# Performance work log

Measured on AMD Instinct MI355X. Metric: run time of the kernel, lower is better.

## Reference

```python
import jax, jax.numpy as jnp
import numpy as np

# dimensions (match init_kwargs / input_specs)
K = 25        # number of observation events
N_PER = 2048  # observations per event
B = 4096      # batch (sample_idx length)
D = 64        # input_dim
NDIM = 8      # memory_dim
H = D * NDIM  # hidden = 512
STEPS = 2     # euler ODE steps between consecutive obs_times
DT = 0.01
LOG_SQRT_2PI = 0.9189385332046727  # log(sqrt(2*pi))


def _xavier(key, shape):
    lim = np.sqrt(6.0 / (shape[0] + shape[1])).astype(np.float32)
    return jax.random.uniform(key, shape, jnp.float32, -lim, lim)


def setup_inputs() -> dict:
    key = jax.random.key(0)
    ks = jax.random.split(key, 10)
    # unique per-event indices (matches torch scatter-assign semantics)
    rng = np.random.RandomState(0)
    batch_idx = jnp.asarray(
        np.stack([rng.permutation(B)[:N_PER] for _ in range(K)]).reshape(-1),
        jnp.int32)
    return {
        "obs_times": jnp.arange(1, K + 1, dtype=jnp.float32) * (STEPS * DT),
        "event_pt": jnp.arange(K + 1, dtype=jnp.int32) * N_PER,
        "sample_idx": jnp.arange(B, dtype=jnp.int32),
        "X": jax.random.normal(ks[0], (K * N_PER, D), jnp.float32),
        "M": (jax.random.uniform(ks[1], (K * N_PER, D)) < 0.8).astype(jnp.float32),
        "batch_idx": batch_idx,
        # ODEFunc: Linear(H,H) -> Tanh -> Linear(H,H)
        "W_ode1": _xavier(ks[2], (H, H)), "b_ode1": jnp.zeros((H,), jnp.float32),
        "W_ode2": _xavier(ks[3], (H, H)), "b_ode2": jnp.zeros((H,), jnp.float32),
        # GRUCell(D, H)
        "W_ih": _xavier(ks[4], (3 * H, D)), "W_hh": _xavier(ks[5], (3 * H, H)),
        "b_ih": jnp.zeros((3 * H,), jnp.float32), "b_hh": jnp.zeros((3 * H,), jnp.float32),
        # p_model: Linear(H,H) -> ReLU -> (dropout=0) -> Linear(H, 2D)
        "Wp1": _xavier(ks[6], (H, H)), "bp1": jnp.zeros((H,), jnp.float32),
        "Wp2": _xavier(ks[7], (2 * D, H)), "bp2": jnp.zeros((2 * D,), jnp.float32),
    }


def reference(obs_times, event_pt, sample_idx, X, M, batch_idx,
              W_ode1, b_ode1, W_ode2, b_ode2,
              W_ih, W_hh, b_ih, b_hh, Wp1, bp1, Wp2, bp2):
    Xr = X.reshape(K, N_PER, D)
    Mr = M.reshape(K, N_PER, D)
    idx = batch_idx.reshape(K, N_PER)

    def ode_func(h):  # Linear -> Tanh -> Linear
        return jnp.tanh(h @ W_ode1.T + b_ode1) @ W_ode2.T + b_ode2

    def gru(x, h):  # torch GRUCell
        gi = x @ W_ih.T + b_ih
        gh = h @ W_hh.T + b_hh
        i_r, i_z, i_n = jnp.split(gi, 3, axis=1)
        h_r, h_z, h_n = jnp.split(gh, 3, axis=1)
        r = jax.nn.sigmoid(i_r + h_r)
        z = jax.nn.sigmoid(i_z + h_z)
        n = jnp.tanh(i_n + r * h_n)
        return (1.0 - z) * n + z * h

    def event_step(carry, inp):
        h, loss, m_tot = carry
        X_obs, M_obs, i_obs = inp
        # euler odeint over [0, dt], STEPS times to reach obs_time
        for _ in range(STEPS):
            h = h + DT * ode_func(h)
        # likelihood head on all samples, gather observed ones
        p = jax.nn.relu(h @ Wp1.T + bp1) @ Wp2.T + bp2       # [B, 2D]
        p_obs = p[i_obs]                                      # [N_PER, 2D]
        mean, logvar = jnp.split(p_obs, 2, axis=1)
        sigma = jnp.exp(0.5 * logvar)
        error = (X_obs - mean) / sigma
        losses = 0.5 * ((error * error + logvar + 2.0 * LOG_SQRT_2PI) * M_obs)
        # GRU update only on observed indices (scatter)
        h = h.at[i_obs].set(gru(X_obs, h[i_obs]))
        return (h, loss + losses.sum(), m_tot + M_obs.sum()), None

    h0 = jnp.zeros((B, H), jnp.float32)
    (h, loss, m_tot), _ = jax.lax.scan(event_step, (h0, jnp.float32(0.0), jnp.float32(0.0)), (Xr, Mr, idx))
    return (loss / m_tot, jnp.float32(0.0))
```

## Files before the change

### kernel.cpp

```cpp
#include <hip/hip_runtime.h>
#include <cstdint>
#include <cstddef>

#define BATCH 4096
#define DIM 64
#define HID 512
#define NPER 2048
#define KEV 25
#define DT_C 0.01f
#define LOG_SQRT_2PI_C 0.9189385332046727f

typedef __attribute__((ext_vector_type(8))) short short8;
typedef __attribute__((ext_vector_type(4))) float f32x4;

#define MFMA(a, b, c) __builtin_amdgcn_mfma_f32_16x16x32_bf16(a, b, c, 0, 0, 0)
#define BARRIER() __builtin_amdgcn_s_barrier()
#define SCHED0()  __builtin_amdgcn_sched_barrier(0)

__device__ __forceinline__ ushort f2bf(float f) {
    uint32_t u = __float_as_uint(f);
    u += 0x7FFF + ((u >> 16) & 1);
    return (ushort)(u >> 16);
}
__device__ __forceinline__ float sigmoidf_(float x) { return 1.0f / (1.0f + expf(-x)); }

__device__ __forceinline__ void gload_lds16(const ushort* g, ushort* l) {
    __builtin_amdgcn_global_load_lds(
        (const __attribute__((address_space(1))) void*)g,
        (__attribute__((address_space(3))) void*)l, 16, 0, 0);
}
__device__ __forceinline__ void wait_vm(int n) {
    if (n == 4)      asm volatile("s_waitcnt vmcnt(4)" ::: "memory");
    else if (n == 6) asm volatile("s_waitcnt vmcnt(6)" ::: "memory");
    else             asm volatile("s_waitcnt vmcnt(0)" ::: "memory");
}

__device__ __forceinline__ short8 frag64(const ushort* lds, int row, int ks, int lane) {
    int slot = ((ks << 2) + (lane >> 4)) ^ (row & 7);
    return *(const short8*)&lds[row * 64 + slot * 8];
}

__device__ __forceinline__ void gemm64_pipe(
    ushort* A0, ushort* A1, ushort* B0, ushort* B1,
    int w, int lane, int wr, int wc,
    const ushort* gA0, const ushort* gA1,
    const ushort* gB0, const ushort* gB1,
    const ushort* tA0, const ushort* tA1,
    const ushort* tB0, const ushort* tB1,
    int NT, bool tailToX, f32x4 acc[2][2], f32x4 accX[2][2])
{
    auto stage = [&](int b, int p) {
        ushort* A = b ? A1 : A0; ushort* B = b ? B1 : B0;
        if (p < 8) {
            gload_lds16(gA0 + (size_t)p * 64, &A[(w * 16) * 64]);
            gload_lds16(gA1 + (size_t)p * 64, &A[(w * 16 + 8) * 64]);
            gload_lds16(gB0 + (size_t)p * 64, &B[(w * 16) * 64]);
            gload_lds16(gB1 + (size_t)p * 64, &B[(w * 16 + 8) * 64]);
        } else {
            gload_lds16(tA0, &A[(w * 16) * 64]);
            gload_lds16(tA1, &A[(w * 16 + 8) * 64]);
            gload_lds16(tB0, &B[(w * 16) * 64]);
            gload_lds16(tB1, &B[(w * 16 + 8) * 64]);
        }
    };
    stage(0, 0);
    stage(1, 1);
    for (int t = 0; t < NT; ++t) {
        wait_vm((t + 1 < NT) ? 4 : 0);
        BARRIER();
        SCHED0();
        const ushort* Ab = (t & 1) ? A1 : A0;
        const ushort* Bb = (t & 1) ? B1 : B0;
        short8 af[2][2], bf[2][2];
        #pragma unroll
        for (int mi = 0; mi < 2; ++mi) {
            int r = wr * 32 + mi * 16 + (lane & 15);
            af[mi][0] = frag64(Ab, r, 0, lane);
            af[mi][1] = frag64(Ab, r, 1, lane);
        }
        #pragma unroll
        for (int ni = 0; ni < 2; ++ni) {
            int c = wc * 32 + ni * 16 + (lane & 15);
            bf[ni][0] = frag64(Bb, c, 0, lane);
            bf[ni][1] = frag64(Bb, c, 1, lane);
        }
        const bool toX = tailToX && (t == 8);
        #pragma unroll
        for (int ks = 0; ks < 2; ++ks)
            #pragma unroll
            for (int mi = 0; mi < 2; ++mi)
                #pragma unroll
                for (int ni = 0; ni < 2; ++ni) {
                    f32x4& a = toX ? accX[mi][ni] : acc[mi][ni];
                    a = MFMA(af[mi][ks], bf[ni][ks], a);
                }
        SCHED0();
        BARRIER();
        if (t + 2 < NT) stage(t & 1, t + 2);
    }
}

__global__ __launch_bounds__(256) void fuse1(
    const ushort* __restrict__ hb, const ushort* __restrict__ W1,
    const float* __restrict__ b1, ushort* __restrict__ tbb,
    const ushort* __restrict__ hgb, const ushort* __restrict__ Wp1,
    const float* __restrict__ bp1, ushort* __restrict__ qb, int mode)
{
    __shared__ __align__(16) ushort Alds[2][4096];
    __shared__ __align__(16) ushort Blds[2][4096];
    const int tid = threadIdx.x, lane = tid & 63, w = tid >> 6;
    const int wr = w >> 1, wc = w & 1;
    const int srow = lane >> 3, sg = ((lane & 7) ^ srow) << 3;
    const int bid = blockIdx.x;

    bool isQ; int b;
    if (mode == 2)        { isQ = true;  b = bid; }
    else if (bid < 512)   { isQ = false; b = bid; }
    else                  { isQ = true;  b = bid - 512; }
    const ushort* A = isQ ? hgb : hb;
    const ushort* W = isQ ? Wp1 : W1;
    const float* bias = isQ ? bp1 : b1;
    const int r0 = (b >> 3) * 64, c0 = (b & 7) * 64;

    f32x4 acc[2][2] = {}; f32x4 accX[2][2];
    gemm64_pipe(Alds[0], Alds[1], Blds[0], Blds[1], w, lane, wr, wc,
        A + (size_t)(r0 + w * 16 + srow) * HID + sg,
        A + (size_t)(r0 + w * 16 + 8 + srow) * HID + sg,
        W + (size_t)(c0 + w * 16 + srow) * HID + sg,
        W + (size_t)(c0 + w * 16 + 8 + srow) * HID + sg,
        nullptr, nullptr, nullptr, nullptr, 8, false, acc, accX);

    #pragma unroll
    for (int mi = 0; mi < 2; ++mi)
        #pragma unroll
        for (int ni = 0; ni < 2; ++ni) {
            const int c = c0 + wc * 32 + ni * 16 + (lane & 15);
            const float bv = bias[c];
            #pragma unroll
            for (int ii = 0; ii < 4; ++ii) {
                const int r = r0 + wr * 32 + mi * 16 + ((lane >> 4) << 2) + ii;
                const size_t o = (size_t)r * HID + c;
                float v = acc[mi][ni][ii] + bv;
                if (!isQ) tbb[o] = f2bf(tanhf(v));
                else      qb[o]  = f2bf(fmaxf(v, 0.0f));
            }
        }
}

__global__ __launch_bounds__(256) void fuse2(
    const ushort* __restrict__ tbb, const ushort* __restrict__ W2,
    const float* __restrict__ b2, float* __restrict__ h, ushort* __restrict__ hb,
    const ushort* __restrict__ qb, const ushort* __restrict__ Wp2,
    const float* __restrict__ bp2, const float* __restrict__ Xp,
    const float* __restrict__ Mp, float* __restrict__ sums, int mode)
{
    __shared__ __align__(16) ushort smem[24576];
    const int tid = threadIdx.x, lane = tid & 63, w = tid >> 6;
    const int wr = w >> 1, wc = w & 1;
    const int srow = lane >> 3, sg = ((lane & 7) ^ srow) << 3;
    const int bid = blockIdx.x;

    bool isP; int b;
    if (mode == 2)      { isP = true;  b = bid; }
    else if (bid < 512) { isP = false; b = bid; }
    else                { isP = true;  b = bid - 512; }

    if (!isP) {
        const int r0 = (b >> 3) * 64, c0 = (b & 7) * 64;
        ushort* A0 = smem;        ushort* A1 = smem + 4096;
        ushort* B0 = smem + 8192; ushort* B1 = smem + 12288;
        f32x4 acc[2][2] = {}; f32x4 accX[2][2];
        gemm64_pipe(A0, A1, B0, B1, w, lane, wr, wc,
            tbb + (size_t)(r0 + w * 16 + srow) * HID + sg,
            tbb + (size_t)(r0 + w * 16 + 8 + srow) * HID + sg,
            W2 + (size_t)(c0 + w * 16 + srow) * HID + sg,
            W2 + (size_t)(c0 + w * 16 + 8 + srow) * HID + sg,
            nullptr, nullptr, nullptr, nullptr, 8, false, acc, accX);
        #pragma unroll
        for (int mi = 0; mi < 2; ++mi)
            #pragma unroll
            for (int ni = 0; ni < 2; ++ni) {
                const int c = c0 + wc * 32 + ni * 16 + (lane & 15);
                const float bv = b2[c];
                #pragma unroll
                for (int ii = 0; ii < 4; ++ii) {
                    const int r = r0 + wr * 32 + mi * 16 + ((lane >> 4) << 2) + ii;
                    const size_t o = (size_t)r * HID + c;
                    float nh = h[o] + DT_C * (acc[mi][ni][ii] + bv);
                    h[o] = nh; hb[o] = f2bf(nh);
                }
            }
        return;
    }

    ushort* A0 = smem;        ushort* A1 = smem + 4096;
    ushort* B0 = smem + 8192; ushort* B1 = smem + 16384;
    const int r0t = b * 64;
    const int arow = w * 16 + srow;

    auto stage = [&](int bb, int k0) {
        ushort* A = bb ? A1 : A0; ushort* B = bb ? B1 : B0;
        gload_lds16(qb + (size_t)(r0t + arow) * HID + k0 + sg, &A[(w * 16) * 64]);
        gload_lds16(qb + (size_t)(r0t + arow + 8) * HID + k0 + sg, &A[(w * 16 + 8) * 64]);
        #pragma unroll
        for (int j = 0; j < 4; ++j) {
            int g = w * 4 + j;
            int rw = g * 8 + srow;
            gload_lds16(Wp2 + (size_t)rw * HID + k0 + (((lane & 7) ^ (rw & 7)) << 3),
                        &B[g * 8 * 64]);
        }
    };
    f32x4 acc[2][4] = {};
    stage(0, 0);
    stage(1, 64);
    for (int t = 0; t < 8; ++t) {
        wait_vm((t < 7) ? 6 : 0);
        BARRIER();
        SCHED0();
        const ushort* Ab = (t & 1) ? A1 : A0;
        const ushort* Bb = (t & 1) ? B1 : B0;
        short8 af[2][2], bf[4][2];
        #pragma unroll
        for (int mi = 0; mi < 2; ++mi) {
            int r = wr * 32 + mi * 16 + (lane & 15);
            af[mi][0] = frag64(Ab, r, 0, lane);
            af[mi][1] = frag64(Ab, r, 1, lane);
        }
        #pragma unroll
        for (int ni = 0; ni < 4; ++ni) {
            int c = wc * 64 + ni * 16 + (lane & 15);
            bf[ni][0] = frag64(Bb, c, 0, lane);
            bf[ni][1] = frag64(Bb, c, 1, lane);
        }
        #pragma unroll
        for (int ks = 0; ks < 2; ++ks)
            #pragma unroll
            for (int mi = 0; mi < 2; ++mi)
                #pragma unroll
                for (int ni = 0; ni < 4; ++ni)
                    acc[mi][ni] = MFMA(af[mi][ks], bf[ni][ks], acc[mi][ni]);
        SCHED0();
        BARRIER();
        if (t + 2 < 8) stage(t & 1, (t + 2) * 64);
    }

    float* Plds = (float*)smem;
    #pragma unroll
    for (int mi = 0; mi < 2; ++mi)
        #pragma unroll
        for (int ni = 0; ni < 4; ++ni) {
            int c = wc * 64 + ni * 16 + (lane & 15);
            float bv = bp2[c];
            #pragma unroll
            for (int ii = 0; ii < 4; ++ii) {
                int r = wr * 32 + mi * 16 + ((lane >> 4) << 2) + ii;
                Plds[r * 128 + c] = acc[mi][ni][ii] + bv;
            }
        }
    __syncthreads();

    float local = 0.0f;
    for (int t = tid; t < 64 * 64; t += 256) {
        int r = t >> 6, jj = t & 63;
        float mean = Plds[r * 128 + jj];
        float lv   = Plds[r * 128 + 64 + jj];
        int g = r0t + r;
        float err = (Xp[(size_t)g * 64 + jj] - mean) * expf(-0.5f * lv);
        local += 0.5f * (err * err + lv + 2.0f * LOG_SQRT_2PI_C) * Mp[(size_t)g * 64 + jj];
    }
    #pragma unroll
    for (int o = 32; o > 0; o >>= 1) local += __shfl_down(local, o);
    if (lane == 0) atomicAdd(sums, local);
}

__global__ __launch_bounds__(256) void fuse5(
    const ushort* __restrict__ hb, const ushort* __restrict__ Xbk,
    const int* __restrict__ idx,
    const ushort* __restrict__ Whh, const ushort* __restrict__ Wih,
    const float* __restrict__ bih, const float* __restrict__ bhh,
    float* __restrict__ rz, float* __restrict__ nh_, float* __restrict__ nx_,
    ushort* __restrict__ hgb)
{
    __shared__ __align__(16) ushort Alds[2][4096];
    __shared__ __align__(16) ushort Blds[2][4096];
    const int tid = threadIdx.x, lane = tid & 63, w = tid >> 6;
    const int wr = w >> 1, wc = w & 1;
    const int srow = lane >> 3, sg = ((lane & 7) ^ srow) << 3;
    const int bid = blockIdx.x;

    if (bid >= 768) {
        int t0 = (bid - 768) * 256 + tid;
        #pragma unroll
        for (int i = 0; i < 32; ++i) {
            int v = t0 + i * 4096;
            int row = v >> 6, c8 = (v & 63) << 3;
            size_t src = (size_t)idx[row] * HID + c8;
            size_t dst = (size_t)row * HID + c8;
            *(ushort4*)&hgb[dst]     = *(const ushort4*)&hb[src];
            *(ushort4*)&hgb[dst + 4] = *(const ushort4*)&hb[src + 4];
        }
        return;
    }

    int r0t, c0;
    const ushort *Bh, *Bx;
    bool tailX;
    if (bid < 512) { r0t = (bid >> 4) * 64; c0 = (bid & 15) * 64; Bh = Whh; Bx = Wih; tailX = false; }
    else { int t3 = bid - 512; r0t = (t3 >> 3) * 64; c0 = (t3 & 7) * 64;
           Bh = Whh + (size_t)1024 * HID; Bx = Wih + (size_t)1024 * DIM; tailX = true; }

    const int ar0 = r0t + w * 16 + srow, ar1 = r0t + w * 16 + 8 + srow;
    f32x4 acc[2][2] = {}, accX[2][2] = {};
    gemm64_pipe(Alds[0], Alds[1], Blds[0], Blds[1], w, lane, wr, wc,
        hb + (size_t)idx[ar0] * HID + sg,
        hb + (size_t)idx[ar1] * HID + sg,
        Bh + (size_t)(c0 + w * 16 + srow) * HID + sg,
        Bh + (size_t)(c0 + w * 16 + 8 + srow) * HID + sg,
        Xbk + (size_t)ar0 * DIM + sg,
        Xbk + (size_t)ar1 * DIM + sg,
        Bx + (size_t)(c0 + w * 16 + srow) * DIM + sg,
        Bx + (size_t)(c0 + w * 16 + 8 + srow) * DIM + sg,
        9, tailX, acc, accX);

    #pragma unroll
    for (int mi = 0; mi < 2; ++mi)
        #pragma unroll
        for (int ni = 0; ni < 2; ++ni) {
            const int c = c0 + wc * 32 + ni * 16 + (lane & 15);
            #pragma unroll
            for (int ii = 0; ii < 4; ++ii) {
                const int iobs = r0t + wr * 32 + mi * 16 + ((lane >> 4) << 2) + ii;
                if (!tailX) {
                    rz[(size_t)iobs * 1024 + c] =
                        sigmoidf_(acc[mi][ni][ii] + bih[c] + bhh[c]);
                } else {
                    nh_[(size_t)iobs * HID + c] = acc[mi][ni][ii] + bhh[1024 + c];
                    nx_[(size_t)iobs * HID + c] = accX[mi][ni][ii] + bih[1024 + c];
                }
            }
        }
}

__global__ __launch_bounds__(256) void combine_kernel(
    const float* __restrict__ rz, const float* __restrict__ nh_,
    const float* __restrict__ nx_, const int* __restrict__ idx,
    float* __restrict__ h, ushort* __restrict__ hb)
{
    int t = blockIdx.x * 256 + threadIdx.x;
    #pragma unroll
    for (int i = 0; i < 4; ++i) {
        int v = t + i * 65536;
        int row = v >> 7, j4 = (v & 127) << 2;
        float4 rr = *(const float4*)&rz[(size_t)row * 1024 + j4];
        float4 zz = *(const float4*)&rz[(size_t)row * 1024 + 512 + j4];
        float4 hn = *(const float4*)&nh_[(size_t)row * HID + j4];
        float4 xn = *(const float4*)&nx_[(size_t)row * HID + j4];
        size_t o = (size_t)idx[row] * HID + j4;
        float4 hv = *(const float4*)&h[o];
        float4 res; ushort4 ob;
        #define C1(c) { float n = tanhf(xn.c + rr.c * hn.c); \
                        res.c = (1.0f - zz.c) * n + zz.c * hv.c; ob.c = f2bf(res.c); }
        C1(x) C1(y) C1(z) C1(w)
        #undef C1
        *(float4*)&h[o] = res;
        *(ushort4*)&hb[o] = ob;
    }
}

__device__ __forceinline__ void block_atomic_sum(float v, float* acc) {
    __shared__ float red[4];
    #pragma unroll
    for (int off = 32; off > 0; off >>= 1) v += __shfl_down(v, off);
    int lane = threadIdx.x & 63, wid = threadIdx.x >> 6;
    if (lane == 0) red[wid] = v;
    __syncthreads();
    if (threadIdx.x == 0) atomicAdd(acc, red[0] + red[1] + red[2] + red[3]);
}

__global__ __launch_bounds__(256) void f2b4_kernel(
    const float* __restrict__ s, ushort* __restrict__ d, int n4)
{
    int t = blockIdx.x * 256 + threadIdx.x;
    if (t >= n4) return;
    float4 v = ((const float4*)s)[t];
    ushort4 o; o.x = f2bf(v.x); o.y = f2bf(v.y); o.z = f2bf(v.z); o.w = f2bf(v.w);
    ((ushort4*)d)[t] = o;
}

__global__ __launch_bounds__(256) void msum_kernel(
    const float* __restrict__ M, int n, float* __restrict__ m_acc)
{
    float v = 0.0f;
    for (int t = blockIdx.x * 256 + threadIdx.x; t < n; t += gridDim.x * 256)
        v += M[t];
    block_atomic_sum(v, m_acc);
}

__global__ void finalize_kernel(const float* __restrict__ sums, float* __restrict__ out) {
    if (threadIdx.x == 0) { out[0] = sums[0] / sums[1]; out[1] = 0.0f; }
}

extern "C" void kernel_launch(void* const* d_in, const int* in_sizes, int n_in,
                              void* d_out, int out_size, void* d_ws, size_t ws_size,
                              hipStream_t stream) {
    const float* X      = (const float*)d_in[3];
    const float* M      = (const float*)d_in[4];
    const int* batch_idx= (const int*)  d_in[5];
    const float* W_ode1 = (const float*)d_in[6];
    const float* b_ode1 = (const float*)d_in[7];
    const float* W_ode2 = (const float*)d_in[8];
    const float* b_ode2 = (const float*)d_in[9];
    const float* W_ih   = (const float*)d_in[10];
    const float* W_hh   = (const float*)d_in[11];
    const float* b_ih   = (const float*)d_in[12];
    const float* b_hh   = (const float*)d_in[13];
    const float* Wp1    = (const float*)d_in[14];
    const float* bp1    = (const float*)d_in[15];
    const float* Wp2    = (const float*)d_in[16];
    const float* bp2    = (const float*)d_in[17];
    float* out = (float*)d_out;

    float* ws    = (float*)d_ws;
    float* h     = ws;
    float* rz    = h   + (size_t)BATCH * HID;
    float* nh_   = rz  + (size_t)NPER * 1024;
    float* nx_   = nh_ + (size_t)NPER * HID;
    float* sums  = nx_ + (size_t)NPER * HID;
    ushort* hb   = (ushort*)(sums + 16);
    ushort* tbb  = hb  + (size_t)BATCH * HID;
    ushort* qb   = tbb + (size_t)BATCH * HID;
    ushort* hgb  = qb  + (size_t)NPER * HID;
    ushort* Xb   = hgb + (size_t)NPER * HID;
    ushort* W1b  = Xb  + (size_t)KEV * NPER * DIM;
    ushort* W2b  = W1b + (size_t)HID * HID;
    ushort* Wp1b = W2b + (size_t)HID * HID;
    ushort* Wp2b = Wp1b + (size_t)HID * HID;
    ushort* Wihb = Wp2b + (size_t)2 * DIM * HID;
    ushort* Whhb = Wihb + (size_t)3 * HID * DIM;

    hipMemsetAsync(h,    0, (size_t)BATCH * HID * sizeof(float), stream);
    hipMemsetAsync(hb,   0, (size_t)BATCH * HID * sizeof(ushort), stream);
    hipMemsetAsync(sums, 0, 2 * sizeof(float), stream);

    dim3 blk(256);
    auto cvt = [&](const float* s, ushort* d, size_t n) {
        f2b4_kernel<<<dim3((unsigned)((n / 4 + 255) / 256)), blk, 0, stream>>>(s, d, (int)(n / 4));
    };
    cvt(W_ode1, W1b,  (size_t)HID * HID);
    cvt(W_ode2, W2b,  (size_t)HID * HID);
    cvt(Wp1,    Wp1b, (size_t)HID * HID);
    cvt(Wp2,    Wp2b, (size_t)2 * DIM * HID);
    cvt(W_ih,   Wihb, (size_t)3 * HID * DIM);
    cvt(W_hh,   Whhb, (size_t)3 * HID * HID);
    cvt(X,      Xb,   (size_t)KEV * NPER * DIM);

    msum_kernel<<<1024, blk, 0, stream>>>(M, KEV * NPER * DIM, sums + 1);

    for (int k = 0; k < KEV; ++k) {
        const ushort* Xbk = Xb + (size_t)k * NPER * DIM;
        const int*   idxk = batch_idx + (size_t)k * NPER;
        const float* Xp = X + (size_t)(k > 0 ? k - 1 : 0) * NPER * DIM;
        const float* Mp = M + (size_t)(k > 0 ? k - 1 : 0) * NPER * DIM;
        const int m1 = (k > 0) ? 1 : 0;

        fuse1<<<dim3(m1 ? 768 : 512), blk, 0, stream>>>(
            hb, W1b, b_ode1, tbb, hgb, Wp1b, bp1, qb, m1);
        fuse2<<<dim3(m1 ? 544 : 512), blk, 0, stream>>>(
            tbb, W2b, b_ode2, h, hb, qb, Wp2b, bp2, Xp, Mp, sums, m1);
        fuse1<<<dim3(512), blk, 0, stream>>>(
            hb, W1b, b_ode1, tbb, hgb, Wp1b, bp1, qb, 0);
        fuse2<<<dim3(512), blk, 0, stream>>>(
            tbb, W2b, b_ode2, h, hb, qb, Wp2b, bp2, Xp, Mp, sums, 0);
        fuse5<<<dim3(784), blk, 0, stream>>>(
            hb, Xbk, idxk, Whhb, Wihb, b_ih, b_hh, rz, nh_, nx_, hgb);
        combine_kernel<<<dim3(256), blk, 0, stream>>>(rz, nh_, nx_, idxk, h, hb);
    }

    {
        const float* Xp = X + (size_t)(KEV - 1) * NPER * DIM;
        const float* Mp = M + (size_t)(KEV - 1) * NPER * DIM;
        fuse1<<<dim3(256), blk, 0, stream>>>(
            hb, W1b, b_ode1, tbb, hgb, Wp1b, bp1, qb, 2);
        fuse2<<<dim3(32), blk, 0, stream>>>(
            tbb, W2b, b_ode2, h, hb, qb, Wp2b, bp2, Xp, Mp, sums, 2);
    }

    finalize_kernel<<<1, 64, 0, stream>>>(sums, out);
}
```

Measured before the change: 1.997 ms.

## Fuse GRU gate GEMMs with combine, scatter gathered state in ODE epilogue, BK=128 GEMM

```diff
diff --git a/kernel.cpp b/kernel.cpp
--- a/kernel.cpp
+++ b/kernel.cpp
@@ -30,8 +30,9 @@
         (__attribute__((address_space(3))) void*)l, 16, 0, 0);
 }
 __device__ __forceinline__ void wait_vm(int n) {
-    if (n == 4)      asm volatile("s_waitcnt vmcnt(4)" ::: "memory");
+    if (n == 8)      asm volatile("s_waitcnt vmcnt(8)" ::: "memory");
     else if (n == 6) asm volatile("s_waitcnt vmcnt(6)" ::: "memory");
+    else if (n == 4) asm volatile("s_waitcnt vmcnt(4)" ::: "memory");
     else             asm volatile("s_waitcnt vmcnt(0)" ::: "memory");
 }
 
@@ -39,64 +40,65 @@
     int slot = ((ks << 2) + (lane >> 4)) ^ (row & 7);
     return *(const short8*)&lds[row * 64 + slot * 8];
 }
-
-__device__ __forceinline__ void gemm64_pipe(
+__device__ __forceinline__ short8 frag128(const ushort* lds, int row, int ks, int lane) {
+    int slot = ((ks << 2) + (lane >> 4)) ^ (row & 7);
+    return *(const short8*)&lds[row * 128 + slot * 8];
+}
+
+__device__ __forceinline__ void stage128(
+    const ushort* g, int row0, int k0, int w, int lane, ushort* lds)
+{
+    #pragma unroll
+    for (int gg = 0; gg < 4; ++gg) {
+        int row = row0 + w * 16 + gg * 4 + (lane >> 4);
+        int slot = (lane & 15) ^ (row & 7);
+        gload_lds16(g + (size_t)row * HID + k0 + slot * 8,
+                    &lds[(w * 16 + gg * 4) * 128]);
+    }
+}
+
+__device__ __forceinline__ void gemm_bk128(
     ushort* A0, ushort* A1, ushort* B0, ushort* B1,
     int w, int lane, int wr, int wc,
-    const ushort* gA0, const ushort* gA1,
-    const ushort* gB0, const ushort* gB1,
-    const ushort* tA0, const ushort* tA1,
-    const ushort* tB0, const ushort* tB1,
-    int NT, bool tailToX, f32x4 acc[2][2], f32x4 accX[2][2])
-{
-    auto stage = [&](int b, int p) {
-        ushort* A = b ? A1 : A0; ushort* B = b ? B1 : B0;
-        if (p < 8) {
-            gload_lds16(gA0 + (size_t)p * 64, &A[(w * 16) * 64]);
-            gload_lds16(gA1 + (size_t)p * 64, &A[(w * 16 + 8) * 64]);
-            gload_lds16(gB0 + (size_t)p * 64, &B[(w * 16) * 64]);
-            gload_lds16(gB1 + (size_t)p * 64, &B[(w * 16 + 8) * 64]);
-        } else {
-            gload_lds16(tA0, &A[(w * 16) * 64]);
-            gload_lds16(tA1, &A[(w * 16 + 8) * 64]);
-            gload_lds16(tB0, &B[(w * 16) * 64]);
-            gload_lds16(tB1, &B[(w * 16 + 8) * 64]);
-        }
-    };
-    stage(0, 0);
-    stage(1, 1);
-    for (int t = 0; t < NT; ++t) {
-        wait_vm((t + 1 < NT) ? 4 : 0);
+    const ushort* Ag, int arow0, const ushort* Bg, int brow0,
+    f32x4 acc[2][2])
+{
+    stage128(Ag, arow0, 0, w, lane, A0);
+    stage128(Bg, brow0, 0, w, lane, B0);
+    stage128(Ag, arow0, 128, w, lane, A1);
+    stage128(Bg, brow0, 128, w, lane, B1);
+    for (int t = 0; t < 4; ++t) {
+        wait_vm((t < 3) ? 8 : 0);
         BARRIER();
         SCHED0();
         const ushort* Ab = (t & 1) ? A1 : A0;
         const ushort* Bb = (t & 1) ? B1 : B0;
-        short8 af[2][2], bf[2][2];
+        short8 af[2][4], bf[2][4];
         #pragma unroll
         for (int mi = 0; mi < 2; ++mi) {
             int r = wr * 32 + mi * 16 + (lane & 15);
-            af[mi][0] = frag64(Ab, r, 0, lane);
-            af[mi][1] = frag64(Ab, r, 1, lane);
+            #pragma unroll
+            for (int ks = 0; ks < 4; ++ks) af[mi][ks] = frag128(Ab, r, ks, lane);
         }
         #pragma unroll
         for (int ni = 0; ni < 2; ++ni) {
             int c = wc * 32 + ni * 16 + (lane & 15);
-            bf[ni][0] = frag64(Bb, c, 0, lane);
-            bf[ni][1] = frag64(Bb, c, 1, lane);
-        }
-        const bool toX = tailToX && (t == 8);
-        #pragma unroll
-        for (int ks = 0; ks < 2; ++ks)
+            #pragma unroll
+            for (int ks = 0; ks < 4; ++ks) bf[ni][ks] = frag128(Bb, c, ks, lane);
+        }
+        #pragma unroll
+        for (int ks = 0; ks < 4; ++ks)
             #pragma unroll
             for (int mi = 0; mi < 2; ++mi)
                 #pragma unroll
-                for (int ni = 0; ni < 2; ++ni) {
-                    f32x4& a = toX ? accX[mi][ni] : acc[mi][ni];
-                    a = MFMA(af[mi][ks], bf[ni][ks], a);
-                }
-        SCHED0();
-        BARRIER();
-        if (t + 2 < NT) stage(t & 1, t + 2);
+                for (int ni = 0; ni < 2; ++ni)
+                    acc[mi][ni] = MFMA(af[mi][ks], bf[ni][ks], acc[mi][ni]);
+        SCHED0();
+        BARRIER();
+        if (t + 2 < 4) {
+            stage128(Ag, arow0, (t + 2) * 128, w, lane, (t & 1) ? A1 : A0);
+            stage128(Bg, brow0, (t + 2) * 128, w, lane, (t & 1) ? B1 : B0);
+        }
     }
 }
 
@@ -106,29 +108,24 @@
     const ushort* __restrict__ hgb, const ushort* __restrict__ Wp1,
     const float* __restrict__ bp1, ushort* __restrict__ qb, int mode)
 {
-    __shared__ __align__(16) ushort Alds[2][4096];
-    __shared__ __align__(16) ushort Blds[2][4096];
+    __shared__ __align__(16) ushort smem[32768];
+    ushort* A0 = smem;         ushort* A1 = smem + 8192;
+    ushort* B0 = smem + 16384; ushort* B1 = smem + 24576;
     const int tid = threadIdx.x, lane = tid & 63, w = tid >> 6;
     const int wr = w >> 1, wc = w & 1;
-    const int srow = lane >> 3, sg = ((lane & 7) ^ srow) << 3;
     const int bid = blockIdx.x;
 
     bool isQ; int b;
-    if (mode == 2)        { isQ = true;  b = bid; }
-    else if (bid < 512)   { isQ = false; b = bid; }
-    else                  { isQ = true;  b = bid - 512; }
+    if (mode == 2)      { isQ = true;  b = bid; }
+    else if (bid < 512) { isQ = false; b = bid; }
+    else                { isQ = true;  b = bid - 512; }
     const ushort* A = isQ ? hgb : hb;
     const ushort* W = isQ ? Wp1 : W1;
     const float* bias = isQ ? bp1 : b1;
     const int r0 = (b >> 3) * 64, c0 = (b & 7) * 64;
 
-    f32x4 acc[2][2] = {}; f32x4 accX[2][2];
-    gemm64_pipe(Alds[0], Alds[1], Blds[0], Blds[1], w, lane, wr, wc,
-        A + (size_t)(r0 + w * 16 + srow) * HID + sg,
-        A + (size_t)(r0 + w * 16 + 8 + srow) * HID + sg,
-        W + (size_t)(c0 + w * 16 + srow) * HID + sg,
-        W + (size_t)(c0 + w * 16 + 8 + srow) * HID + sg,
-        nullptr, nullptr, nullptr, nullptr, 8, false, acc, accX);
+    f32x4 acc[2][2] = {};
+    gemm_bk128(A0, A1, B0, B1, w, lane, wr, wc, A, r0, W, c0, acc);
 
     #pragma unroll
     for (int mi = 0; mi < 2; ++mi)
@@ -150,14 +147,14 @@
 __global__ __launch_bounds__(256) void fuse2(
     const ushort* __restrict__ tbb, const ushort* __restrict__ W2,
     const float* __restrict__ b2, float* __restrict__ h, ushort* __restrict__ hb,
+    const int* __restrict__ inv, ushort* __restrict__ hgb,
     const ushort* __restrict__ qb, const ushort* __restrict__ Wp2,
     const float* __restrict__ bp2, const float* __restrict__ Xp,
     const float* __restrict__ Mp, float* __restrict__ sums, int mode)
 {
-    __shared__ __align__(16) ushort smem[24576];
+    __shared__ __align__(16) ushort smem[32768];
     const int tid = threadIdx.x, lane = tid & 63, w = tid >> 6;
     const int wr = w >> 1, wc = w & 1;
-    const int srow = lane >> 3, sg = ((lane & 7) ^ srow) << 3;
     const int bid = blockIdx.x;
 
     bool isP; int b;
@@ -166,16 +163,11 @@
     else                { isP = true;  b = bid - 512; }
 
     if (!isP) {
+        ushort* A0 = smem;         ushort* A1 = smem + 8192;
+        ushort* B0 = smem + 16384; ushort* B1 = smem + 24576;
         const int r0 = (b >> 3) * 64, c0 = (b & 7) * 64;
-        ushort* A0 = smem;        ushort* A1 = smem + 4096;
-        ushort* B0 = smem + 8192; ushort* B1 = smem + 12288;
-        f32x4 acc[2][2] = {}; f32x4 accX[2][2];
-        gemm64_pipe(A0, A1, B0, B1, w, lane, wr, wc,
-            tbb + (size_t)(r0 + w * 16 + srow) * HID + sg,
-            tbb + (size_t)(r0 + w * 16 + 8 + srow) * HID + sg,
-            W2 + (size_t)(c0 + w * 16 + srow) * HID + sg,
-            W2 + (size_t)(c0 + w * 16 + 8 + srow) * HID + sg,
-            nullptr, nullptr, nullptr, nullptr, 8, false, acc, accX);
+        f32x4 acc[2][2] = {};
+        gemm_bk128(A0, A1, B0, B1, w, lane, wr, wc, tbb, r0, W2, c0, acc);
         #pragma unroll
         for (int mi = 0; mi < 2; ++mi)
             #pragma unroll
@@ -187,7 +179,13 @@
                     const int r = r0 + wr * 32 + mi * 16 + ((lane >> 4) << 2) + ii;
                     const size_t o = (size_t)r * HID + c;
                     float nh = h[o] + DT_C * (acc[mi][ni][ii] + bv);
-                    h[o] = nh; hb[o] = f2bf(nh);
+                    h[o] = nh;
+                    ushort bv16 = f2bf(nh);
+                    hb[o] = bv16;
+                    if (inv) {
+                        int iv = inv[r];
+                        if (iv >= 0) hgb[(size_t)iv * HID + c] = bv16;
+                    }
                 }
             }
         return;
@@ -195,6 +193,7 @@
 
     ushort* A0 = smem;        ushort* A1 = smem + 4096;
     ushort* B0 = smem + 8192; ushort* B1 = smem + 16384;
+    const int srow = lane >> 3, sg = ((lane & 7) ^ srow) << 3;
     const int r0t = b * 64;
     const int arow = w * 16 + srow;
 
@@ -273,98 +272,143 @@
     if (lane == 0) atomicAdd(sums, local);
 }
 
-__global__ __launch_bounds__(256) void fuse5(
-    const ushort* __restrict__ hb, const ushort* __restrict__ Xbk,
+__global__ __launch_bounds__(256) void gru_all(
+    const ushort* __restrict__ hgb, const ushort* __restrict__ Xbk,
     const int* __restrict__ idx,
     const ushort* __restrict__ Whh, const ushort* __restrict__ Wih,
     const float* __restrict__ bih, const float* __restrict__ bhh,
-    float* __restrict__ rz, float* __restrict__ nh_, float* __restrict__ nx_,
-    ushort* __restrict__ hgb)
-{
-    __shared__ __align__(16) ushort Alds[2][4096];
-    __shared__ __align__(16) ushort Blds[2][4096];
+    float* __restrict__ h, ushort* __restrict__ hb)
+{
+    __shared__ __align__(16) ushort smem[32768];
     const int tid = threadIdx.x, lane = tid & 63, w = tid >> 6;
     const int wr = w >> 1, wc = w & 1;
     const int srow = lane >> 3, sg = ((lane & 7) ^ srow) << 3;
     const int bid = blockIdx.x;
-
-    if (bid >= 768) {
-        int t0 = (bid - 768) * 256 + tid;
-        #pragma unroll
-        for (int i = 0; i < 32; ++i) {
-            int v = t0 + i * 4096;
-            int row = v >> 6, c8 = (v & 63) << 3;
-            size_t src = (size_t)idx[row] * HID + c8;
-            size_t dst = (size_t)row * HID + c8;
-            *(ushort4*)&hgb[dst]     = *(const ushort4*)&hb[src];
-            *(ushort4*)&hgb[dst + 4] = *(const ushort4*)&hb[src + 4];
-        }
-        return;
-    }
-
-    int r0t, c0;
-    const ushort *Bh, *Bx;
-    bool tailX;
-    if (bid < 512) { r0t = (bid >> 4) * 64; c0 = (bid & 15) * 64; Bh = Whh; Bx = Wih; tailX = false; }
-    else { int t3 = bid - 512; r0t = (t3 >> 3) * 64; c0 = (t3 & 7) * 64;
-           Bh = Whh + (size_t)1024 * HID; Bx = Wih + (size_t)1024 * DIM; tailX = true; }
-
-    const int ar0 = r0t + w * 16 + srow, ar1 = r0t + w * 16 + 8 + srow;
-    f32x4 acc[2][2] = {}, accX[2][2] = {};
-    gemm64_pipe(Alds[0], Alds[1], Blds[0], Blds[1], w, lane, wr, wc,
-        hb + (size_t)idx[ar0] * HID + sg,
-        hb + (size_t)idx[ar1] * HID + sg,
-        Bh + (size_t)(c0 + w * 16 + srow) * HID + sg,
-        Bh + (size_t)(c0 + w * 16 + 8 + srow) * HID + sg,
-        Xbk + (size_t)ar0 * DIM + sg,
-        Xbk + (size_t)ar1 * DIM + sg,
-        Bx + (size_t)(c0 + w * 16 + srow) * DIM + sg,
-        Bx + (size_t)(c0 + w * 16 + 8 + srow) * DIM + sg,
-        9, tailX, acc, accX);
+    const int r0t = (bid >> 3) * 64, c0 = (bid & 7) * 64;
+
+    auto stage = [&](int b, int p) {
+        ushort* A = smem + b * 4096;
+        if (p < 8) {
+            gload_lds16(hgb + (size_t)(r0t + w * 16 + srow) * HID + p * 64 + sg,
+                        &A[(w * 16) * 64]);
+            gload_lds16(hgb + (size_t)(r0t + w * 16 + 8 + srow) * HID + p * 64 + sg,
+                        &A[(w * 16 + 8) * 64]);
+            #pragma unroll
+            for (int g = 0; g < 3; ++g) {
+                ushort* B = smem + 8192 + (b * 3 + g) * 4096;
+                gload_lds16(Whh + (size_t)(g * 512 + c0 + w * 16 + srow) * HID + p * 64 + sg,
+                            &B[(w * 16) * 64]);
+                gload_lds16(Whh + (size_t)(g * 512 + c0 + w * 16 + 8 + srow) * HID + p * 64 + sg,
+                            &B[(w * 16 + 8) * 64]);
+            }
+        } else {
+            gload_lds16(Xbk + (size_t)(r0t + w * 16 + srow) * DIM + sg, &A[(w * 16) * 64]);
+            gload_lds16(Xbk + (size_t)(r0t + w * 16 + 8 + srow) * DIM + sg, &A[(w * 16 + 8) * 64]);
+            #pragma unroll
+            for (int g = 0; g < 3; ++g) {
+                ushort* B = smem + 8192 + (b * 3 + g) * 4096;
+                gload_lds16(Wih + (size_t)(g * 512 + c0 + w * 16 + srow) * DIM + sg,
+                            &B[(w * 16) * 64]);
+                gload_lds16(Wih + (size_t)(g * 512 + c0 + w * 16 + 8 + srow) * DIM + sg,
+                            &B[(w * 16 + 8) * 64]);
+            }
+        }
+    };
+
+    f32x4 aR[2][2] = {}, aZ[2][2] = {}, aNh[2][2] = {}, aNx[2][2] = {};
+    stage(0, 0);
+    stage(1, 1);
+    for (int t = 0; t < 8; ++t) {
+        wait_vm(8);
+        BARRIER();
+        SCHED0();
+        const ushort* Ab = smem + (t & 1) * 4096;
+        short8 af[2][2];
+        #pragma unroll
+        for (int mi = 0; mi < 2; ++mi) {
+            int r = wr * 32 + mi * 16 + (lane & 15);
+            af[mi][0] = frag64(Ab, r, 0, lane);
+            af[mi][1] = frag64(Ab, r, 1, lane);
+        }
+        #pragma unroll
+        for (int g = 0; g < 3; ++g) {
+            const ushort* Bb = smem + 8192 + ((t & 1) * 3 + g) * 4096;
+            short8 bf[2][2];
+            #pragma unroll
+            for (int ni = 0; ni < 2; ++ni) {
+                int c = wc * 32 + ni * 16 + (lane & 15);
+                bf[ni][0] = frag64(Bb, c, 0, lane);
+                bf[ni][1] = frag64(Bb, c, 1, lane);
+            }
+            #pragma unroll
+            for (int ks = 0; ks < 2; ++ks)
+                #pragma unroll
+                for (int mi = 0; mi < 2; ++mi)
+                    #pragma unroll
+                    for (int ni = 0; ni < 2; ++ni) {
+                        f32x4& a = (g == 0) ? aR[mi][ni] : (g == 1) ? aZ[mi][ni] : aNh[mi][ni];
+                        a = MFMA(af[mi][ks], bf[ni][ks], a);
+                    }
+        }
+        SCHED0();
+        BARRIER();
+        if (t + 2 < 9) stage(t & 1, t + 2);
+    }
+    {
+        wait_vm(0);
+        BARRIER();
+        SCHED0();
+        const ushort* Ab = smem;
+        short8 af[2][2];
+        #pragma unroll
+        for (int mi = 0; mi < 2; ++mi) {
+            int r = wr * 32 + mi * 16 + (lane & 15);
+            af[mi][0] = frag64(Ab, r, 0, lane);
+            af[mi][1] = frag64(Ab, r, 1, lane);
+        }
+        #pragma unroll
+        for (int g = 0; g < 3; ++g) {
+            const ushort* Bb = smem + 8192 + g * 4096;
+            short8 bf[2][2];
+            #pragma unroll
+            for (int ni = 0; ni < 2; ++ni) {
+                int c = wc * 32 + ni * 16 + (lane & 15);
+                bf[ni][0] = frag64(Bb, c, 0, lane);
+                bf[ni][1] = frag64(Bb, c, 1, lane);
+            }
+            #pragma unroll
+            for (int ks = 0; ks < 2; ++ks)
+                #pragma unroll
+                for (int mi = 0; mi < 2; ++mi)
+                    #pragma unroll
+                    for (int ni = 0; ni < 2; ++ni) {
+                        f32x4& a = (g == 0) ? aR[mi][ni] : (g == 1) ? aZ[mi][ni] : aNx[mi][ni];
+                        a = MFMA(af[mi][ks], bf[ni][ks], a);
+                    }
+        }
+    }
 
     #pragma unroll
     for (int mi = 0; mi < 2; ++mi)
         #pragma unroll
         for (int ni = 0; ni < 2; ++ni) {
             const int c = c0 + wc * 32 + ni * 16 + (lane & 15);
+            const float bR = bih[c] + bhh[c];
+            const float bZ = bih[512 + c] + bhh[512 + c];
+            const float bNx = bih[1024 + c], bNh = bhh[1024 + c];
             #pragma unroll
             for (int ii = 0; ii < 4; ++ii) {
                 const int iobs = r0t + wr * 32 + mi * 16 + ((lane >> 4) << 2) + ii;
-                if (!tailX) {
-                    rz[(size_t)iobs * 1024 + c] =
-                        sigmoidf_(acc[mi][ni][ii] + bih[c] + bhh[c]);
-                } else {
-                    nh_[(size_t)iobs * HID + c] = acc[mi][ni][ii] + bhh[1024 + c];
-                    nx_[(size_t)iobs * HID + c] = accX[mi][ni][ii] + bih[1024 + c];
-                }
-            }
-        }
-}
-
-__global__ __launch_bounds__(256) void combine_kernel(
-    const float* __restrict__ rz, const float* __restrict__ nh_,
-    const float* __restrict__ nx_, const int* __restrict__ idx,
-    float* __restrict__ h, ushort* __restrict__ hb)
-{
-    int t = blockIdx.x * 256 + threadIdx.x;
-    #pragma unroll
-    for (int i = 0; i < 4; ++i) {
-        int v = t + i * 65536;
-        int row = v >> 7, j4 = (v & 127) << 2;
-        float4 rr = *(const float4*)&rz[(size_t)row * 1024 + j4];
-        float4 zz = *(const float4*)&rz[(size_t)row * 1024 + 512 + j4];
-        float4 hn = *(const float4*)&nh_[(size_t)row * HID + j4];
-        float4 xn = *(const float4*)&nx_[(size_t)row * HID + j4];
-        size_t o = (size_t)idx[row] * HID + j4;
-        float4 hv = *(const float4*)&h[o];
-        float4 res; ushort4 ob;
-        #define C1(c) { float n = tanhf(xn.c + rr.c * hn.c); \
-                        res.c = (1.0f - zz.c) * n + zz.c * hv.c; ob.c = f2bf(res.c); }
-        C1(x) C1(y) C1(z) C1(w)
-        #undef C1
-        *(float4*)&h[o] = res;
-        *(ushort4*)&hb[o] = ob;
-    }
+                const int gr = idx[iobs];
+                float r = sigmoidf_(aR[mi][ni][ii] + bR);
+                float z = sigmoidf_(aZ[mi][ni][ii] + bZ);
+                float n = tanhf(aNx[mi][ni][ii] + bNx + r * (aNh[mi][ni][ii] + bNh));
+                const size_t o = (size_t)gr * HID + c;
+                float nh = (1.0f - z) * n + z * h[o];
+                h[o] = nh;
+                hb[o] = f2bf(nh);
+            }
+        }
 }
 
 __device__ __forceinline__ void block_atomic_sum(float v, float* acc) {
@@ -394,6 +438,15 @@
     for (int t = blockIdx.x * 256 + threadIdx.x; t < n; t += gridDim.x * 256)
         v += M[t];
     block_atomic_sum(v, m_acc);
+}
+
+__global__ __launch_bounds__(256) void inv_scatter(
+    const int* __restrict__ bidx, int* __restrict__ inv)
+{
+    int t = blockIdx.x * 256 + threadIdx.x;
+    if (t >= KEV * NPER) return;
+    int e = t >> 11, i = t & (NPER - 1);
+    inv[(size_t)e * BATCH + bidx[t]] = i;
 }
 
 __global__ void finalize_kernel(const float* __restrict__ sums, float* __restrict__ out) {
@@ -422,11 +475,9 @@
 
     float* ws    = (float*)d_ws;
     float* h     = ws;
-    float* rz    = h   + (size_t)BATCH * HID;
-    float* nh_   = rz  + (size_t)NPER * 1024;
-    float* nx_   = nh_ + (size_t)NPER * HID;
-    float* sums  = nx_ + (size_t)NPER * HID;
-    ushort* hb   = (ushort*)(sums + 16);
+    float* sums  = h + (size_t)BATCH * HID;
+    int*   inv   = (int*)(sums + 16);
+    ushort* hb   = (ushort*)(inv + (size_t)KEV * BATCH);
     ushort* tbb  = hb  + (size_t)BATCH * HID;
     ushort* qb   = tbb + (size_t)BATCH * HID;
     ushort* hgb  = qb  + (size_t)NPER * HID;
@@ -441,6 +492,7 @@
     hipMemsetAsync(h,    0, (size_t)BATCH * HID * sizeof(float), stream);
     hipMemsetAsync(hb,   0, (size_t)BATCH * HID * sizeof(ushort), stream);
     hipMemsetAsync(sums, 0, 2 * sizeof(float), stream);
+    hipMemsetAsync(inv,  0xFF, (size_t)KEV * BATCH * sizeof(int), stream);
 
     dim3 blk(256);
     auto cvt = [&](const float* s, ushort* d, size_t n) {
@@ -455,10 +507,12 @@
     cvt(X,      Xb,   (size_t)KEV * NPER * DIM);
 
     msum_kernel<<<1024, blk, 0, stream>>>(M, KEV * NPER * DIM, sums + 1);
+    inv_scatter<<<(KEV * NPER + 255) / 256, blk, 0, stream>>>(batch_idx, inv);
 
     for (int k = 0; k < KEV; ++k) {
         const ushort* Xbk = Xb + (size_t)k * NPER * DIM;
         const int*   idxk = batch_idx + (size_t)k * NPER;
+        int* invk = inv + (size_t)k * BATCH;
         const float* Xp = X + (size_t)(k > 0 ? k - 1 : 0) * NPER * DIM;
         const float* Mp = M + (size_t)(k > 0 ? k - 1 : 0) * NPER * DIM;
         const int m1 = (k > 0) ? 1 : 0;
@@ -466,14 +520,15 @@
         fuse1<<<dim3(m1 ? 768 : 512), blk, 0, stream>>>(
             hb, W1b, b_ode1, tbb, hgb, Wp1b, bp1, qb, m1);
         fuse2<<<dim3(m1 ? 544 : 512), blk, 0, stream>>>(
-            tbb, W2b, b_ode2, h, hb, qb, Wp2b, bp2, Xp, Mp, sums, m1);
+            tbb, W2b, b_ode2, h, hb, nullptr, hgb,
+            qb, Wp2b, bp2, Xp, Mp, sums, m1);
         fuse1<<<dim3(512), blk, 0, stream>>>(
             hb, W1b, b_ode1, tbb, hgb, Wp1b, bp1, qb, 0);
         fuse2<<<dim3(512), blk, 0, stream>>>(
-            tbb, W2b, b_ode2, h, hb, qb, Wp2b, bp2, Xp, Mp, sums, 0);
-        fuse5<<<dim3(784), blk, 0, stream>>>(
-            hb, Xbk, idxk, Whhb, Wihb, b_ih, b_hh, rz, nh_, nx_, hgb);
-        combine_kernel<<<dim3(256), blk, 0, stream>>>(rz, nh_, nx_, idxk, h, hb);
+            tbb, W2b, b_ode2, h, hb, invk, hgb,
+            qb, Wp2b, bp2, Xp, Mp, sums, 0);
+        gru_all<<<dim3(256), blk, 0, stream>>>(
+            hgb, Xbk, idxk, Whhb, Wihb, b_ih, b_hh, h, hb);
     }
 
     {
@@ -482,7 +537,8 @@
         fuse1<<<dim3(256), blk, 0, stream>>>(
             hb, W1b, b_ode1, tbb, hgb, Wp1b, bp1, qb, 2);
         fuse2<<<dim3(32), blk, 0, stream>>>(
-            tbb, W2b, b_ode2, h, hb, qb, Wp2b, bp2, Xp, Mp, sums, 2);
+            tbb, W2b, b_ode2, h, hb, nullptr, hgb,
+            qb, Wp2b, bp2, Xp, Mp, sums, 2);
     }
 
     finalize_kernel<<<1, 64, 0, stream>>>(sums, out);
```

Result: faster. 1.930 ms, median of 2 (-3.3%).

## Fuse observed-row gather into ODE epilogue and widen GEMM K-tile to 128

Applied to the files above, without the earlier changes.

```diff
diff --git a/kernel.cpp b/kernel.cpp
--- a/kernel.cpp
+++ b/kernel.cpp
@@ -30,14 +30,76 @@
         (__attribute__((address_space(3))) void*)l, 16, 0, 0);
 }
 __device__ __forceinline__ void wait_vm(int n) {
-    if (n == 4)      asm volatile("s_waitcnt vmcnt(4)" ::: "memory");
+    if (n == 8)      asm volatile("s_waitcnt vmcnt(8)" ::: "memory");
     else if (n == 6) asm volatile("s_waitcnt vmcnt(6)" ::: "memory");
+    else if (n == 4) asm volatile("s_waitcnt vmcnt(4)" ::: "memory");
     else             asm volatile("s_waitcnt vmcnt(0)" ::: "memory");
 }
 
 __device__ __forceinline__ short8 frag64(const ushort* lds, int row, int ks, int lane) {
     int slot = ((ks << 2) + (lane >> 4)) ^ (row & 7);
     return *(const short8*)&lds[row * 64 + slot * 8];
+}
+__device__ __forceinline__ short8 frag128(const ushort* lds, int row, int ks, int lane) {
+    int slot = ((ks << 2) + (lane >> 4)) ^ (row & 7);
+    return *(const short8*)&lds[row * 128 + slot * 8];
+}
+
+__device__ __forceinline__ void stage128(
+    const ushort* g, int row0, int k0, int w, int lane, ushort* lds)
+{
+    #pragma unroll
+    for (int gg = 0; gg < 4; ++gg) {
+        int row = row0 + w * 16 + gg * 4 + (lane >> 4);
+        int slot = (lane & 15) ^ (row & 7);
+        gload_lds16(g + (size_t)row * HID + k0 + slot * 8,
+                    &lds[(w * 16 + gg * 4) * 128]);
+    }
+}
+
+__device__ __forceinline__ void gemm_bk128(
+    ushort* A0, ushort* A1, ushort* B0, ushort* B1,
+    int w, int lane, int wr, int wc,
+    const ushort* Ag, int arow0, const ushort* Bg, int brow0,
+    f32x4 acc[2][2])
+{
+    stage128(Ag, arow0, 0, w, lane, A0);
+    stage128(Bg, brow0, 0, w, lane, B0);
+    stage128(Ag, arow0, 128, w, lane, A1);
+    stage128(Bg, brow0, 128, w, lane, B1);
+    for (int t = 0; t < 4; ++t) {
+        wait_vm((t < 3) ? 8 : 0);
+        BARRIER();
+        SCHED0();
+        const ushort* Ab = (t & 1) ? A1 : A0;
+        const ushort* Bb = (t & 1) ? B1 : B0;
+        short8 af[2][4], bf[2][4];
+        #pragma unroll
+        for (int mi = 0; mi < 2; ++mi) {
+            int r = wr * 32 + mi * 16 + (lane & 15);
+            #pragma unroll
+            for (int ks = 0; ks < 4; ++ks) af[mi][ks] = frag128(Ab, r, ks, lane);
+        }
+        #pragma unroll
+        for (int ni = 0; ni < 2; ++ni) {
+            int c = wc * 32 + ni * 16 + (lane & 15);
+            #pragma unroll
+            for (int ks = 0; ks < 4; ++ks) bf[ni][ks] = frag128(Bb, c, ks, lane);
+        }
+        #pragma unroll
+        for (int ks = 0; ks < 4; ++ks)
+            #pragma unroll
+            for (int mi = 0; mi < 2; ++mi)
+                #pragma unroll
+                for (int ni = 0; ni < 2; ++ni)
+                    acc[mi][ni] = MFMA(af[mi][ks], bf[ni][ks], acc[mi][ni]);
+        SCHED0();
+        BARRIER();
+        if (t + 2 < 4) {
+            stage128(Ag, arow0, (t + 2) * 128, w, lane, (t & 1) ? A1 : A0);
+            stage128(Bg, brow0, (t + 2) * 128, w, lane, (t & 1) ? B1 : B0);
+        }
+    }
 }
 
 __device__ __forceinline__ void gemm64_pipe(
@@ -106,29 +168,24 @@
     const ushort* __restrict__ hgb, const ushort* __restrict__ Wp1,
     const float* __restrict__ bp1, ushort* __restrict__ qb, int mode)
 {
-    __shared__ __align__(16) ushort Alds[2][4096];
-    __shared__ __align__(16) ushort Blds[2][4096];
+    __shared__ __align__(16) ushort smem[32768];
+    ushort* A0 = smem;         ushort* A1 = smem + 8192;
+    ushort* B0 = smem + 16384; ushort* B1 = smem + 24576;
     const int tid = threadIdx.x, lane = tid & 63, w = tid >> 6;
     const int wr = w >> 1, wc = w & 1;
-    const int srow = lane >> 3, sg = ((lane & 7) ^ srow) << 3;
     const int bid = blockIdx.x;
 
     bool isQ; int b;
-    if (mode == 2)        { isQ = true;  b = bid; }
-    else if (bid < 512)   { isQ = false; b = bid; }
-    else                  { isQ = true;  b = bid - 512; }
+    if (mode == 2)      { isQ = true;  b = bid; }
+    else if (bid < 512) { isQ = false; b = bid; }
+    else                { isQ = true;  b = bid - 512; }
     const ushort* A = isQ ? hgb : hb;
     const ushort* W = isQ ? Wp1 : W1;
     const float* bias = isQ ? bp1 : b1;
     const int r0 = (b >> 3) * 64, c0 = (b & 7) * 64;
 
-    f32x4 acc[2][2] = {}; f32x4 accX[2][2];
-    gemm64_pipe(Alds[0], Alds[1], Blds[0], Blds[1], w, lane, wr, wc,
-        A + (size_t)(r0 + w * 16 + srow) * HID + sg,
-        A + (size_t)(r0 + w * 16 + 8 + srow) * HID + sg,
-        W + (size_t)(c0 + w * 16 + srow) * HID + sg,
-        W + (size_t)(c0 + w * 16 + 8 + srow) * HID + sg,
-        nullptr, nullptr, nullptr, nullptr, 8, false, acc, accX);
+    f32x4 acc[2][2] = {};
+    gemm_bk128(A0, A1, B0, B1, w, lane, wr, wc, A, r0, W, c0, acc);
 
     #pragma unroll
     for (int mi = 0; mi < 2; ++mi)
@@ -150,14 +207,14 @@
 __global__ __launch_bounds__(256) void fuse2(
     const ushort* __restrict__ tbb, const ushort* __restrict__ W2,
     const float* __restrict__ b2, float* __restrict__ h, ushort* __restrict__ hb,
+    const int* __restrict__ inv, ushort* __restrict__ hgb,
     const ushort* __restrict__ qb, const ushort* __restrict__ Wp2,
     const float* __restrict__ bp2, const float* __restrict__ Xp,
     const float* __restrict__ Mp, float* __restrict__ sums, int mode)
 {
-    __shared__ __align__(16) ushort smem[24576];
+    __shared__ __align__(16) ushort smem[32768];
     const int tid = threadIdx.x, lane = tid & 63, w = tid >> 6;
     const int wr = w >> 1, wc = w & 1;
-    const int srow = lane >> 3, sg = ((lane & 7) ^ srow) << 3;
     const int bid = blockIdx.x;
 
     bool isP; int b;
@@ -166,16 +223,11 @@
     else                { isP = true;  b = bid - 512; }
 
     if (!isP) {
+        ushort* A0 = smem;         ushort* A1 = smem + 8192;
+        ushort* B0 = smem + 16384; ushort* B1 = smem + 24576;
         const int r0 = (b >> 3) * 64, c0 = (b & 7) * 64;
-        ushort* A0 = smem;        ushort* A1 = smem + 4096;
-        ushort* B0 = smem + 8192; ushort* B1 = smem + 12288;
-        f32x4 acc[2][2] = {}; f32x4 accX[2][2];
-        gemm64_pipe(A0, A1, B0, B1, w, lane, wr, wc,
-            tbb + (size_t)(r0 + w * 16 + srow) * HID + sg,
-            tbb + (size_t)(r0 + w * 16 + 8 + srow) * HID + sg,
-            W2 + (size_t)(c0 + w * 16 + srow) * HID + sg,
-            W2 + (size_t)(c0 + w * 16 + 8 + srow) * HID + sg,
-            nullptr, nullptr, nullptr, nullptr, 8, false, acc, accX);
+        f32x4 acc[2][2] = {};
+        gemm_bk128(A0, A1, B0, B1, w, lane, wr, wc, tbb, r0, W2, c0, acc);
         #pragma unroll
         for (int mi = 0; mi < 2; ++mi)
             #pragma unroll
@@ -187,7 +239,13 @@
                     const int r = r0 + wr * 32 + mi * 16 + ((lane >> 4) << 2) + ii;
                     const size_t o = (size_t)r * HID + c;
                     float nh = h[o] + DT_C * (acc[mi][ni][ii] + bv);
-                    h[o] = nh; hb[o] = f2bf(nh);
+                    h[o] = nh;
+                    ushort bv16 = f2bf(nh);
+                    hb[o] = bv16;
+                    if (inv) {
+                        int iv = inv[r];
+                        if (iv >= 0) hgb[(size_t)iv * HID + c] = bv16;
+                    }
                 }
             }
         return;
@@ -195,6 +253,7 @@
 
     ushort* A0 = smem;        ushort* A1 = smem + 4096;
     ushort* B0 = smem + 8192; ushort* B1 = smem + 16384;
+    const int srow = lane >> 3, sg = ((lane & 7) ^ srow) << 3;
     const int r0t = b * 64;
     const int arow = w * 16 + srow;
 
@@ -274,12 +333,10 @@
 }
 
 __global__ __launch_bounds__(256) void fuse5(
-    const ushort* __restrict__ hb, const ushort* __restrict__ Xbk,
-    const int* __restrict__ idx,
+    const ushort* __restrict__ hgb, const ushort* __restrict__ Xbk,
     const ushort* __restrict__ Whh, const ushort* __restrict__ Wih,
     const float* __restrict__ bih, const float* __restrict__ bhh,
-    float* __restrict__ rz, float* __restrict__ nh_, float* __restrict__ nx_,
-    ushort* __restrict__ hgb)
+    float* __restrict__ rz, float* __restrict__ nh_, float* __restrict__ nx_)
 {
     __shared__ __align__(16) ushort Alds[2][4096];
     __shared__ __align__(16) ushort Blds[2][4096];
@@ -288,20 +345,6 @@
     const int srow = lane >> 3, sg = ((lane & 7) ^ srow) << 3;
     const int bid = blockIdx.x;
 
-    if (bid >= 768) {
-        int t0 = (bid - 768) * 256 + tid;
-        #pragma unroll
-        for (int i = 0; i < 32; ++i) {
-            int v = t0 + i * 4096;
-            int row = v >> 6, c8 = (v & 63) << 3;
-            size_t src = (size_t)idx[row] * HID + c8;
-            size_t dst = (size_t)row * HID + c8;
-            *(ushort4*)&hgb[dst]     = *(const ushort4*)&hb[src];
-            *(ushort4*)&hgb[dst + 4] = *(const ushort4*)&hb[src + 4];
-        }
-        return;
-    }
-
     int r0t, c0;
     const ushort *Bh, *Bx;
     bool tailX;
@@ -312,8 +355,8 @@
     const int ar0 = r0t + w * 16 + srow, ar1 = r0t + w * 16 + 8 + srow;
     f32x4 acc[2][2] = {}, accX[2][2] = {};
     gemm64_pipe(Alds[0], Alds[1], Blds[0], Blds[1], w, lane, wr, wc,
-        hb + (size_t)idx[ar0] * HID + sg,
-        hb + (size_t)idx[ar1] * HID + sg,
+        hgb + (size_t)ar0 * HID + sg,
+        hgb + (size_t)ar1 * HID + sg,
         Bh + (size_t)(c0 + w * 16 + srow) * HID + sg,
         Bh + (size_t)(c0 + w * 16 + 8 + srow) * HID + sg,
         Xbk + (size_t)ar0 * DIM + sg,
@@ -394,6 +437,15 @@
     for (int t = blockIdx.x * 256 + threadIdx.x; t < n; t += gridDim.x * 256)
         v += M[t];
     block_atomic_sum(v, m_acc);
+}
+
+__global__ __launch_bounds__(256) void inv_scatter(
+    const int* __restrict__ bidx, int* __restrict__ inv)
+{
+    int t = blockIdx.x * 256 + threadIdx.x;
+    if (t >= KEV * NPER) return;
+    int e = t >> 11, i = t & (NPER - 1);
+    inv[(size_t)e * BATCH + bidx[t]] = i;
 }
 
 __global__ void finalize_kernel(const float* __restrict__ sums, float* __restrict__ out) {
@@ -426,7 +478,8 @@
     float* nh_   = rz  + (size_t)NPER * 1024;
     float* nx_   = nh_ + (size_t)NPER * HID;
     float* sums  = nx_ + (size_t)NPER * HID;
-    ushort* hb   = (ushort*)(sums + 16);
+    int*   inv   = (int*)(sums + 16);
+    ushort* hb   = (ushort*)(inv + (size_t)KEV * BATCH);
     ushort* tbb  = hb  + (size_t)BATCH * HID;
     ushort* qb   = tbb + (size_t)BATCH * HID;
     ushort* hgb  = qb  + (size_t)NPER * HID;
@@ -441,6 +494,7 @@
     hipMemsetAsync(h,    0, (size_t)BATCH * HID * sizeof(float), stream);
     hipMemsetAsync(hb,   0, (size_t)BATCH * HID * sizeof(ushort), stream);
     hipMemsetAsync(sums, 0, 2 * sizeof(float), stream);
+    hipMemsetAsync(inv,  0xFF, (size_t)KEV * BATCH * sizeof(int), stream);
 
     dim3 blk(256);
     auto cvt = [&](const float* s, ushort* d, size_t n) {
@@ -455,10 +509,12 @@
     cvt(X,      Xb,   (size_t)KEV * NPER * DIM);
 
     msum_kernel<<<1024, blk, 0, stream>>>(M, KEV * NPER * DIM, sums + 1);
+    inv_scatter<<<(KEV * NPER + 255) / 256, blk, 0, stream>>>(batch_idx, inv);
 
     for (int k = 0; k < KEV; ++k) {
         const ushort* Xbk = Xb + (size_t)k * NPER * DIM;
         const int*   idxk = batch_idx + (size_t)k * NPER;
+        int* invk = inv + (size_t)k * BATCH;
         const float* Xp = X + (size_t)(k > 0 ? k - 1 : 0) * NPER * DIM;
         const float* Mp = M + (size_t)(k > 0 ? k - 1 : 0) * NPER * DIM;
         const int m1 = (k > 0) ? 1 : 0;
@@ -466,13 +522,15 @@
         fuse1<<<dim3(m1 ? 768 : 512), blk, 0, stream>>>(
             hb, W1b, b_ode1, tbb, hgb, Wp1b, bp1, qb, m1);
         fuse2<<<dim3(m1 ? 544 : 512), blk, 0, stream>>>(
-            tbb, W2b, b_ode2, h, hb, qb, Wp2b, bp2, Xp, Mp, sums, m1);
+            tbb, W2b, b_ode2, h, hb, nullptr, hgb,
+            qb, Wp2b, bp2, Xp, Mp, sums, m1);
         fuse1<<<dim3(512), blk, 0, stream>>>(
             hb, W1b, b_ode1, tbb, hgb, Wp1b, bp1, qb, 0);
         fuse2<<<dim3(512), blk, 0, stream>>>(
-            tbb, W2b, b_ode2, h, hb, qb, Wp2b, bp2, Xp, Mp, sums, 0);
-        fuse5<<<dim3(784), blk, 0, stream>>>(
-            hb, Xbk, idxk, Whhb, Wihb, b_ih, b_hh, rz, nh_, nx_, hgb);
+            tbb, W2b, b_ode2, h, hb, invk, hgb,
+            qb, Wp2b, bp2, Xp, Mp, sums, 0);
+        fuse5<<<dim3(768), blk, 0, stream>>>(
+            hgb, Xbk, Whhb, Wihb, b_ih, b_hh, rz, nh_, nx_);
         combine_kernel<<<dim3(256), blk, 0, stream>>>(rz, nh_, nx_, idxk, h, hb);
     }
 
@@ -482,7 +540,8 @@
         fuse1<<<dim3(256), blk, 0, stream>>>(
             hb, W1b, b_ode1, tbb, hgb, Wp1b, bp1, qb, 2);
         fuse2<<<dim3(32), blk, 0, stream>>>(
-            tbb, W2b, b_ode2, h, hb, qb, Wp2b, bp2, Xp, Mp, sums, 2);
+            tbb, W2b, b_ode2, h, hb, nullptr, hgb,
+            qb, Wp2b, bp2, Xp, Mp, sums, 2);
     }
 
     finalize_kernel<<<1, 64, 0, stream>>>(sums, out);
```

Result: slower. 2.148 ms (+7.5%).
